# Performance work log

Measured on AMD Instinct MI355X. Metric: run time of the kernel, lower is better.

## Reference

```python
import jax, jax.numpy as jnp
import numpy as np
from jax import lax

B, N, S, C_IN, C_OUT = 4, 16384, 4096, 256, 256


def setup_inputs() -> dict:
    key = jax.random.key(0)
    k1, k2, k3, k4 = jax.random.split(key, 4)
    xyz1 = jax.random.normal(k1, (B, 3, N), dtype=jnp.float32)
    xyz2 = jax.random.normal(k2, (B, 3, S), dtype=jnp.float32)
    points2 = jax.random.normal(k3, (B, C_IN, S), dtype=jnp.float32)
    W = jax.random.normal(k4, (C_OUT, C_IN), dtype=jnp.float32) * (1.0 / np.sqrt(C_IN))
    b = jnp.zeros((C_OUT,), dtype=jnp.float32)
    return {"xyz1": xyz1, "xyz2": xyz2, "points2": points2, "W": W, "b": b}


def reference(xyz1, xyz2, points2, W, b):
    # channel-first -> channel-last
    p1 = jnp.transpose(xyz1, (0, 2, 1))        # [B, N, 3]
    p2 = jnp.transpose(xyz2, (0, 2, 1))        # [B, S, 3]
    f2 = jnp.transpose(points2, (0, 2, 1))     # [B, S, C]
    Bn, Nn, _ = p1.shape
    Cn = f2.shape[-1]
    # squared pairwise distances [B, N, S]
    d = (-2.0 * jnp.einsum('bnc,bsc->bns', p1, p2)
         + jnp.sum(p1 * p1, axis=-1)[:, :, None]
         + jnp.sum(p2 * p2, axis=-1)[:, None, :])
    # 3 nearest neighbors (smallest distances) -- equivalent to sort + slice :3
    neg_d3, idx = lax.top_k(-d, 3)             # [B, N, 3]
    d3 = -neg_d3
    recip = 1.0 / (d3 + 1e-8)
    weight = recip / jnp.sum(recip, axis=-1, keepdims=True)   # [B, N, 3]
    # gather neighbor features: [B, N, 3, C]
    gathered = jnp.take_along_axis(
        f2, idx.reshape(Bn, Nn * 3)[..., None], axis=1
    ).reshape(Bn, Nn, 3, Cn)
    interp = jnp.sum(gathered * weight[..., None], axis=2)    # [B, N, C]
    # Conv1d(kernel=1) == per-point linear: [B, C_out, N]
    out = jnp.einsum('bnc,oc->bon', interp, W) + b[None, :, None]
    return out
```

## Files before the change

### kernel.cpp

```cpp
#include <hip/hip_runtime.h>

#define BB 4
#define NN 16384
#define SS 4096
#define CIN 256
#define COUT 256

#define SC 8
#define SCS (SS / SC)
#define SUBS 16
#define SUBL 256
#define KNNB ((NN / 512) * SC * BB)
#define GEMMB ((COUT / 64) * (SS / 64) * BB)
#define RSLVB (BB * NN / 64)

typedef float v2f __attribute__((ext_vector_type(2)));
typedef float v4f __attribute__((ext_vector_type(4)));

__device__ __forceinline__ unsigned short f2bf(float f) {
    unsigned u = __float_as_uint(f);
    u += 0x7FFF + ((u >> 16) & 1);
    return (unsigned short)(u >> 16);
}
__device__ __forceinline__ float bf2f(unsigned short h) {
    return __uint_as_float((unsigned)h << 16);
}

__device__ __forceinline__ void ins_v(float e, float& a, float& b, float& c) {
    float n1 = __builtin_amdgcn_fmed3f(e, a, b);
    float n2 = __builtin_amdgcn_fmed3f(e, b, c);
    a = fminf(a, e); b = n1; c = n2;
}

__device__ __forceinline__ void insert_vi(float e, int gi,
                                          float& k0, float& k1, float& k2,
                                          int& i0, int& i1, int& i2) {
    bool c0 = e < k0, c1 = e < k1, c2 = e < k2;
    float n0 = fminf(e, k0);
    float n1 = __builtin_amdgcn_fmed3f(e, k0, k1);
    float n2 = __builtin_amdgcn_fmed3f(e, k1, k2);
    int t1 = c0 ? i0 : gi;
    int t2 = c1 ? i1 : gi;
    i0 = c0 ? gi : i0;
    i1 = c1 ? t1 : i1;
    i2 = c2 ? t2 : i2;
    k0 = n0; k1 = n1; k2 = n2;
}

__device__ __forceinline__ void ins_lex(float e, int gi,
                                        float& k0, float& k1, float& k2,
                                        int& i0, int& i1, int& i2) {
    bool c0 = (e < k0) || (e == k0 && gi < i0);
    bool c1 = (e < k1) || (e == k1 && gi < i1);
    bool c2 = (e < k2) || (e == k2 && gi < i2);
    float n0 = fminf(e, k0);
    float n1 = __builtin_amdgcn_fmed3f(e, k0, k1);
    float n2 = __builtin_amdgcn_fmed3f(e, k1, k2);
    int t1 = c0 ? i0 : gi;
    int t2 = c1 ? i1 : gi;
    i0 = c0 ? gi : i0;
    i1 = c1 ? t1 : i1;
    i2 = c2 ? t2 : i2;
    k0 = n0; k1 = n1; k2 = n2;
}

__device__ __forceinline__ int ltc(unsigned long long m) {
    return __builtin_amdgcn_mbcnt_hi(
        (unsigned)(m >> 32), __builtin_amdgcn_mbcnt_lo((unsigned)m, 0));
}

#define E2_FROM(p_xy, p_zw, XX, YY, ZZ, e2)                                    \
    do {                                                                       \
        asm("v_pk_fma_f32 %0, %1, %2, %3 op_sel:[0,0,1] op_sel_hi:[0,1,1]"     \
            : "=v"(e2) : "v"(p_zw), "v"(ZZ), "v"(p_zw));                       \
        asm("v_pk_fma_f32 %0, %1, %2, %0 op_sel:[1,0,0] op_sel_hi:[1,1,1]"     \
            : "+v"(e2) : "v"(p_xy), "v"(YY));                                  \
        asm("v_pk_fma_f32 %0, %1, %2, %0 op_sel:[0,0,0] op_sel_hi:[0,1,1]"     \
            : "+v"(e2) : "v"(p_xy), "v"(XX));                                  \
    } while (0)

#define PK_LO(acc, ap, bw)                                                     \
    asm("v_pk_fma_f32 %0, %1, %2, %0 op_sel:[0,0,0] op_sel_hi:[0,1,1]"         \
        : "+v"(acc) : "v"(ap), "v"(bw))
#define PK_HI(acc, ap, bw)                                                     \
    asm("v_pk_fma_f32 %0, %1, %2, %0 op_sel:[1,0,0] op_sel_hi:[1,1,1]"         \
        : "+v"(acc) : "v"(ap), "v"(bw))

__device__ __forceinline__ void knn_phase(int id, int t, float* smem,
                                          const float* __restrict__ xyz1,
                                          const float* __restrict__ xyz2,
                                          float* __restrict__ pv,
                                          float4* __restrict__ cand4) {
    int nb = id & 31;
    int ch = (id >> 5) & 7;
    int b  = id >> 8;
    int s0 = ch * SCS;

    float4* smv = (float4*)smem;
    const float* x2 = xyz2 + (size_t)b * 3 * SS;
    for (int i = t; i < SCS; i += 256) {
        float px = x2[s0 + i];
        float py = x2[SS + s0 + i];
        float pz = x2[2 * SS + s0 + i];
        float4 p4 = make_float4(px, py, pz, fmaf(px, px, fmaf(py, py, pz * pz)));
        smv[i] = p4;
        if (nb == 0) cand4[(size_t)b * SS + s0 + i] = p4;
    }
    __syncthreads();

    int n0  = nb * 512 + t;
    int n1q = n0 + 256;
    const float* xb = xyz1 + (size_t)b * 3 * NN;
    float ax = xb[n0],  ay = xb[NN + n0],  az = xb[2 * NN + n0];
    float bx = xb[n1q], by = xb[NN + n1q], bz = xb[2 * NN + n1q];
    v2f XX = {-2.0f * ax, -2.0f * bx};
    v2f YY = {-2.0f * ay, -2.0f * by};
    v2f ZZ = {-2.0f * az, -2.0f * bz};

#pragma unroll
    for (int half = 0; half < 2; ++half) {
        float A0 = 1e30f, A1 = 1e30f, A2 = 1e30f;
        float B0 = 1e30f, B1 = 1e30f, B2 = 1e30f;
        int sb = half * SUBL;
#pragma unroll 8
        for (int s = sb; s < sb + SUBL; ++s) {
            v4f p = *(const v4f*)(smem + 4 * s);
            v2f pxy = __builtin_shufflevector(p, p, 0, 1);
            v2f pzw = __builtin_shufflevector(p, p, 2, 3);
            v2f e2;
            E2_FROM(pxy, pzw, XX, YY, ZZ, e2);
            float nA1 = __builtin_amdgcn_fmed3f(e2.x, A0, A1);
            float nA2 = __builtin_amdgcn_fmed3f(e2.x, A1, A2);
            A0 = fminf(A0, e2.x); A1 = nA1; A2 = nA2;
            float nB1 = __builtin_amdgcn_fmed3f(e2.y, B0, B1);
            float nB2 = __builtin_amdgcn_fmed3f(e2.y, B1, B2);
            B0 = fminf(B0, e2.y); B1 = nB1; B2 = nB2;
        }
        int sub = ch * 2 + half;
        size_t base = (size_t)(sub * BB + b) * 3;
        pv[(base + 0) * NN + n0]  = A0;
        pv[(base + 1) * NN + n0]  = A1;
        pv[(base + 2) * NN + n0]  = A2;
        pv[(base + 0) * NN + n1q] = B0;
        pv[(base + 1) * NN + n1q] = B1;
        pv[(base + 2) * NN + n1q] = B2;
    }
}

__device__ __forceinline__ void gemm_phase(int g, int t, float* smem,
                                           const float* __restrict__ P,
                                           const float* __restrict__ W,
                                           const float* __restrict__ bias,
                                           unsigned short* __restrict__ Gh) {
    int o0 = (g & 3) * 64;
    int s0 = ((g >> 2) & 63) * 64;
    int b  = g >> 8;
    float* sP = smem;
    float* sW = smem + 1024;
    int i = t & 15;
    int j = t >> 4;

    v2f acc2[4][2];
#pragma unroll
    for (int p = 0; p < 4; ++p) {
        acc2[p][0] = (v2f){0.f, 0.f};
        acc2[p][1] = (v2f){0.f, 0.f};
    }

    const float* Pb = P + (size_t)b * CIN * SS;

    for (int c0 = 0; c0 < CIN; c0 += 16) {
        __syncthreads();
        {
            int col = t & 63;
            int r0r = t >> 6;
#pragma unroll
            for (int r = 0; r < 4; ++r) {
                int row = r0r + r * 4;
                sP[row * 64 + col] = Pb[(size_t)(c0 + row) * SS + s0 + col];
            }
        }
        {
            int cc = t & 15;
            int obase = t >> 4;
#pragma unroll
            for (int r = 0; r < 4; ++r) {
                int oo = obase + 16 * r;
                sW[cc * 68 + oo] = W[(size_t)(o0 + oo) * CIN + c0 + cc];
            }
        }
        __syncthreads();

#pragma unroll
        for (int cc = 0; cc < 16; ++cc) {
            v4f a  = *(const v4f*)&sP[cc * 64 + i * 4];
            v4f bv = *(const v4f*)&sW[cc * 68 + j * 4];
            v2f a01 = __builtin_shufflevector(a, a, 0, 1);
            v2f a23 = __builtin_shufflevector(a, a, 2, 3);
            v2f b01 = __builtin_shufflevector(bv, bv, 0, 1);
            v2f b23 = __builtin_shufflevector(bv, bv, 2, 3);
            PK_LO(acc2[0][0], a01, b01); PK_LO(acc2[0][1], a01, b23);
            PK_HI(acc2[1][0], a01, b01); PK_HI(acc2[1][1], a01, b23);
            PK_LO(acc2[2][0], a23, b01); PK_LO(acc2[2][1], a23, b23);
            PK_HI(acc2[3][0], a23, b01); PK_HI(acc2[3][1], a23, b23);
        }
    }

    float b0 = bias[o0 + j * 4 + 0];
    float b1 = bias[o0 + j * 4 + 1];
    float b2 = bias[o0 + j * 4 + 2];
    float b3 = bias[o0 + j * 4 + 3];
#pragma unroll
    for (int p = 0; p < 4; ++p) {
        ushort4 v;
        v.x = f2bf(acc2[p][0].x + b0);
        v.y = f2bf(acc2[p][0].y + b1);
        v.z = f2bf(acc2[p][1].x + b2);
        v.w = f2bf(acc2[p][1].y + b3);
        size_t off = ((size_t)b * SS + s0 + i * 4 + p) * COUT + o0 + j * 4;
        *(ushort4*)&Gh[off] = v;
    }
}

__global__ __launch_bounds__(256) void k_fused(const float* __restrict__ xyz1,
                                               const float* __restrict__ xyz2,
                                               const float* __restrict__ P,
                                               const float* __restrict__ W,
                                               const float* __restrict__ bias,
                                               unsigned short* __restrict__ Gh,
                                               float* __restrict__ pv,
                                               float4* __restrict__ cand4) {
    __shared__ float smem[2112];
    int bid = blockIdx.x;
    int t   = threadIdx.x;

    if (bid < KNNB) {
        knn_phase(bid, t, smem, xyz1, xyz2, pv, cand4);
    } else {
        gemm_phase(bid - KNNB, t, smem, P, W, bias, Gh);
    }
}

__global__ __launch_bounds__(256) void k_resolve(const float* __restrict__ pv,
                                                 const float* __restrict__ xyz1,
                                                 const float4* __restrict__ cand4,
                                                 float4* __restrict__ wi4,
                                                 int4* __restrict__ gi4) {
    __shared__ float    sv[4][64][3];
    __shared__ float    sj0[16][64];
    __shared__ float    sm2[64];
    __shared__ unsigned smask[64];
    __shared__ float    sq[64][4];
    __shared__ uint2    sl[4][16];
    int bid = blockIdx.x;
    int b   = bid >> 8;
    int n0  = (bid & 255) * 64;
    int t   = threadIdx.x;
    int w   = t >> 6;
    int l   = t & 63;

    const float* xb = xyz1 + (size_t)b * 3 * NN;

    {
        float a0 = 1e30f, a1 = 1e30f, a2 = 1e30f;
#pragma unroll
        for (int i = 0; i < 12; ++i) {
            int sub = w * 4 + i / 3;
            int j   = i % 3;
            float v = pv[((size_t)(sub * BB + b) * 3 + j) * NN + n0 + l];
            if (j == 0) sj0[sub][l] = v;
            ins_v(v, a0, a1, a2);
        }
        sv[w][l][0] = a0; sv[w][l][1] = a1; sv[w][l][2] = a2;
    }
    if (w == 1) {
        float qx = xb[n0 + l], qy = xb[NN + n0 + l], qz = xb[2 * NN + n0 + l];
        sq[l][0] = -2.0f * qx;
        sq[l][1] = -2.0f * qy;
        sq[l][2] = -2.0f * qz;
        sq[l][3] = fmaf(qx, qx, fmaf(qy, qy, qz * qz));
    }
    __syncthreads();

    {
        float m0 = 1e30f, m1 = 1e30f, m2 = 1e30f;
#pragma unroll
        for (int ww = 0; ww < 4; ++ww) {
            ins_v(sv[ww][l][0], m0, m1, m2);
            ins_v(sv[ww][l][1], m0, m1, m2);
            ins_v(sv[ww][l][2], m0, m1, m2);
        }
        unsigned mk = 0;
#pragma unroll
        for (int sub = 0; sub < SUBS; ++sub)
            mk |= (sj0[sub][l] <= m2) ? (1u << sub) : 0u;
        if (w == 0) { sm2[l] = m2; smask[l] = mk; }
    }
    __syncthreads();

    const float4* cb = cand4 + (size_t)b * SS;
    for (int qq = 0; qq < 16; ++qq) {
        int q = w * 16 + qq;
        int n = n0 + q;
        float    m2q = sm2[q];
        unsigned mm  = smask[q];
        float xm2c = sq[q][0], ym2c = sq[q][1], zm2c = sq[q][2];

        float k0 = 1e30f, k1 = 1e30f, k2 = 1e30f;
        int   i0 = 0,     i1 = 0,     i2 = 0;
        unsigned msc = mm;
        while (msc) {
            int sub = __builtin_ctz(msc); msc &= msc - 1;
            int sb = sub * SUBL;
#pragma unroll
            for (int r = 0; r < 4; ++r) {
                int gi = sb + r * 64 + l;
                float4 p = cb[gi];
                float e = fmaf(p.x, xm2c, fmaf(p.y, ym2c, fmaf(p.z, zm2c, p.w)));
                insert_vi(e, gi, k0, k1, k2, i0, i1, i2);
            }
        }

        unsigned long long b0 = __ballot(k0 <= m2q);
        unsigned long long b1 = __ballot(k1 <= m2q);
        unsigned long long b2 = __ballot(k2 <= m2q);
        int p0 = __popcll(b0), p1 = __popcll(b1);
        int cnt3 = p0 + p1 + __popcll(b2);
        float K0 = 1e30f, K1 = 1e30f, K2 = 1e30f;
        int   I0 = 0,     I1 = 0,     I2 = 0;
        if (cnt3 <= 16) {
            if (k0 <= m2q) sl[w][ltc(b0)]           = make_uint2(__float_as_uint(k0), (unsigned)i0);
            if (k1 <= m2q) sl[w][p0 + ltc(b1)]      = make_uint2(__float_as_uint(k1), (unsigned)i1);
            if (k2 <= m2q) sl[w][p0 + p1 + ltc(b2)] = make_uint2(__float_as_uint(k2), (unsigned)i2);
            for (int j = 0; j < cnt3; ++j) {
                uint2 u = sl[w][j];
                ins_lex(__uint_as_float(u.x), (int)u.y, K0, K1, K2, I0, I1, I2);
            }
        } else {
            unsigned mf = mm;
            while (mf) {
                int sub = __builtin_ctz(mf); mf &= mf - 1;
                int sb = sub * SUBL;
                for (int s = 0; s < SUBL; ++s) {
                    float4 p = cb[sb + s];
                    float e = fmaf(p.x, xm2c, fmaf(p.y, ym2c, fmaf(p.z, zm2c, p.w)));
                    ins_lex(e, sb + s, K0, K1, K2, I0, I1, I2);
                }
            }
        }

        if (l == 0) {
            float nrm = sq[q][3];
            float d0 = K0 + nrm, d1 = K1 + nrm, d2 = K2 + nrm;
            float r0 = 1.0f / (d0 + 1e-8f);
            float r1 = 1.0f / (d1 + 1e-8f);
            float r2 = 1.0f / (d2 + 1e-8f);
            float inv = 1.0f / (r0 + r1 + r2);
            size_t oq = (size_t)b * NN + n;
            wi4[oq] = make_float4(r0 * inv, r1 * inv, r2 * inv, 0.f);
            gi4[oq] = make_int4(I0, I1, I2, 0);
        }
    }
}

__global__ __launch_bounds__(256) void k_out(const unsigned short* __restrict__ Gh,
                                             const float4* __restrict__ wi4,
                                             const int4* __restrict__ gi4,
                                             float* __restrict__ out) {
    __shared__ float  tile[64 * 68];
    __shared__ float4 swv[64];
    __shared__ int4   siv[64];
    int bid  = blockIdx.x;
    int x    = bid & 7;
    int b    = x >> 1;
    int local = (bid >> 3) + (x & 1) * 512;
    int nb   = local & 255;
    int oc   = local >> 8;
    int n0   = nb * 64;
    int o0   = oc * 64;
    int t    = threadIdx.x;
    int wave = t >> 6;
    int lane = t & 63;
    int qg   = lane >> 4;
    int c16  = lane & 15;

    if (t < 64) {
        size_t q = (size_t)b * NN + n0 + t;
        swv[t] = wi4[q];
        siv[t] = gi4[q];
    }
    __syncthreads();

    const unsigned short* Gb = Gh + (size_t)b * SS * COUT;

#pragma unroll
    for (int pass = 0; pass < 4; ++pass) {
        int q = pass * 16 + wave * 4 + qg;
        float4 wv = swv[q];
        int4   iv = siv[q];
        int co = o0 + c16 * 4;
        ushort4 a0 = *(const ushort4*)(Gb + (size_t)iv.x * COUT + co);
        ushort4 a1 = *(const ushort4*)(Gb + (size_t)iv.y * COUT + co);
        ushort4 a2 = *(const ushort4*)(Gb + (size_t)iv.z * COUT + co);
        float4 v;
        v.x = fmaf(wv.x, bf2f(a0.x), fmaf(wv.y, bf2f(a1.x), wv.z * bf2f(a2.x)));
        v.y = fmaf(wv.x, bf2f(a0.y), fmaf(wv.y, bf2f(a1.y), wv.z * bf2f(a2.y)));
        v.z = fmaf(wv.x, bf2f(a0.z), fmaf(wv.y, bf2f(a1.z), wv.z * bf2f(a2.z)));
        v.w = fmaf(wv.x, bf2f(a0.w), fmaf(wv.y, bf2f(a1.w), wv.z * bf2f(a2.w)));
        *(float4*)&tile[q * 68 + c16 * 4] = v;
    }
    __syncthreads();

    float* obase = out + ((size_t)b * COUT + o0) * NN + n0 + lane;
#pragma unroll
    for (int g = 0; g < 4; ++g) {
        int c = wave * 16 + g * 4;
        float4 v = *(const float4*)&tile[lane * 68 + c];
        obase[(size_t)(c + 0) * NN] = v.x;
        obase[(size_t)(c + 1) * NN] = v.y;
        obase[(size_t)(c + 2) * NN] = v.z;
        obase[(size_t)(c + 3) * NN] = v.w;
    }
}

extern "C" void kernel_launch(void* const* d_in, const int* in_sizes, int n_in,
                              void* d_out, int out_size, void* d_ws, size_t ws_size,
                              hipStream_t stream) {
    const float* xyz1    = (const float*)d_in[0];
    const float* xyz2    = (const float*)d_in[1];
    const float* points2 = (const float*)d_in[2];
    const float* W       = (const float*)d_in[3];
    const float* bias    = (const float*)d_in[4];
    float* out = (float*)d_out;

    char* ws = (char*)d_ws;
    float*          pv  = (float*)(ws);
    unsigned short* Gh  = (unsigned short*)(ws + 12582912);
    float4*         wi4 = (float4*)(ws + 20971520);
    int4*           gi4 = (int4*)(ws + 22020096);
    float4* cand4 = (float4*)((char*)d_out + 66846720);

    k_fused<<<dim3(KNNB + GEMMB), 256, 0, stream>>>(xyz1, xyz2, points2, W, bias,
                                                    Gh, pv, cand4);
    k_resolve<<<dim3(RSLVB), 256, 0, stream>>>(pv, xyz1, cand4, wi4, gi4);
    k_out<<<dim3(4096), 256, 0, stream>>>(Gh, wi4, gi4, out);
}
```

Measured before the change: 210.4 us.

## Refine KNN pruning mask to 64-candidate subchunks with per-chunk minima

The KNN pass now records the minimum distance for each 64-candidate subchunk, not only per 256-candidate subchunk, and writes these minima into a scratch region of the output buffer. The resolve kernel builds a 64-bit mask of subchunks whose minimum is within the third-best bound, and rescans only those 64-point chunks. The first three chunk loads are issued up front. This cuts the candidates re-examined during resolve, at the cost of extra min tracking in the KNN inner loop and extra global writes and reads of the minima array.

```diff
diff --git a/kernel.cpp b/kernel.cpp
--- a/kernel.cpp
+++ b/kernel.cpp
@@ -10,6 +10,7 @@
 #define SCS (SS / SC)
 #define SUBS 16
 #define SUBL 256
+#define FSUB 64
 #define KNNB ((NN / 512) * SC * BB)
 #define GEMMB ((COUT / 64) * (SS / 64) * BB)
 #define RSLVB (BB * NN / 64)
@@ -90,6 +91,7 @@
                                           const float* __restrict__ xyz1,
                                           const float* __restrict__ xyz2,
                                           float* __restrict__ pv,
+                                          float* __restrict__ pm,
                                           float4* __restrict__ cand4) {
     int nb = id & 31;
     int ch = (id >> 5) & 7;
@@ -122,19 +124,26 @@
         float A0 = 1e30f, A1 = 1e30f, A2 = 1e30f;
         float B0 = 1e30f, B1 = 1e30f, B2 = 1e30f;
         int sb = half * SUBL;
+#pragma unroll
+        for (int k64 = 0; k64 < 4; ++k64) {
+            float mA = 1e30f, mB = 1e30f;
 #pragma unroll 8
-        for (int s = sb; s < sb + SUBL; ++s) {
-            v4f p = *(const v4f*)(smem + 4 * s);
-            v2f pxy = __builtin_shufflevector(p, p, 0, 1);
-            v2f pzw = __builtin_shufflevector(p, p, 2, 3);
-            v2f e2;
-            E2_FROM(pxy, pzw, XX, YY, ZZ, e2);
-            float nA1 = __builtin_amdgcn_fmed3f(e2.x, A0, A1);
-            float nA2 = __builtin_amdgcn_fmed3f(e2.x, A1, A2);
-            A0 = fminf(A0, e2.x); A1 = nA1; A2 = nA2;
-            float nB1 = __builtin_amdgcn_fmed3f(e2.y, B0, B1);
-            float nB2 = __builtin_amdgcn_fmed3f(e2.y, B1, B2);
-            B0 = fminf(B0, e2.y); B1 = nB1; B2 = nB2;
+            for (int s2 = 0; s2 < 64; ++s2) {
+                int s = sb + k64 * 64 + s2;
+                v4f p = *(const v4f*)(smem + 4 * s);
+                v2f pxy = __builtin_shufflevector(p, p, 0, 1);
+                v2f pzw = __builtin_shufflevector(p, p, 2, 3);
+                v2f e2;
+                E2_FROM(pxy, pzw, XX, YY, ZZ, e2);
+                ins_v(e2.x, A0, A1, A2);
+                ins_v(e2.y, B0, B1, B2);
+                mA = fminf(mA, e2.x);
+                mB = fminf(mB, e2.y);
+            }
+            int sub64 = ch * 8 + half * 4 + k64;
+            size_t pb = (size_t)(sub64 * BB + b) * NN;
+            pm[pb + n0]  = mA;
+            pm[pb + n1q] = mB;
         }
         int sub = ch * 2 + half;
         size_t base = (size_t)(sub * BB + b) * 3;
@@ -229,27 +238,29 @@
                                                const float* __restrict__ bias,
                                                unsigned short* __restrict__ Gh,
                                                float* __restrict__ pv,
+                                               float* __restrict__ pm,
                                                float4* __restrict__ cand4) {
     __shared__ float smem[2112];
     int bid = blockIdx.x;
     int t   = threadIdx.x;
 
     if (bid < KNNB) {
-        knn_phase(bid, t, smem, xyz1, xyz2, pv, cand4);
+        knn_phase(bid, t, smem, xyz1, xyz2, pv, pm, cand4);
     } else {
         gemm_phase(bid - KNNB, t, smem, P, W, bias, Gh);
     }
 }
 
 __global__ __launch_bounds__(256) void k_resolve(const float* __restrict__ pv,
+                                                 const float* __restrict__ pm,
                                                  const float* __restrict__ xyz1,
                                                  const float4* __restrict__ cand4,
                                                  float4* __restrict__ wi4,
                                                  int4* __restrict__ gi4) {
     __shared__ float    sv[4][64][3];
-    __shared__ float    sj0[16][64];
+    __shared__ float    pmv[FSUB][65];
     __shared__ float    sm2[64];
-    __shared__ unsigned smask[64];
+    __shared__ unsigned long long smask[64];
     __shared__ float    sq[64][4];
     __shared__ uint2    sl[4][16];
     int bid = blockIdx.x;
@@ -268,10 +279,14 @@
             int sub = w * 4 + i / 3;
             int j   = i % 3;
             float v = pv[((size_t)(sub * BB + b) * 3 + j) * NN + n0 + l];
-            if (j == 0) sj0[sub][l] = v;
             ins_v(v, a0, a1, a2);
         }
         sv[w][l][0] = a0; sv[w][l][1] = a1; sv[w][l][2] = a2;
+    }
+#pragma unroll
+    for (int i = 0; i < 16; ++i) {
+        int sub = w * 16 + i;
+        pmv[sub][l] = pm[(size_t)(sub * BB + b) * NN + n0 + l];
     }
     if (w == 1) {
         float qx = xb[n0 + l], qy = xb[NN + n0 + l], qz = xb[2 * NN + n0 + l];
@@ -290,10 +305,10 @@
             ins_v(sv[ww][l][1], m0, m1, m2);
             ins_v(sv[ww][l][2], m0, m1, m2);
         }
-        unsigned mk = 0;
-#pragma unroll
-        for (int sub = 0; sub < SUBS; ++sub)
-            mk |= (sj0[sub][l] <= m2) ? (1u << sub) : 0u;
+        unsigned long long mk = 0;
+#pragma unroll
+        for (int sub = 0; sub < FSUB; ++sub)
+            mk |= (pmv[sub][l] <= m2) ? (1ull << sub) : 0ull;
         if (w == 0) { sm2[l] = m2; smask[l] = mk; }
     }
     __syncthreads();
@@ -302,22 +317,42 @@
     for (int qq = 0; qq < 16; ++qq) {
         int q = w * 16 + qq;
         int n = n0 + q;
-        float    m2q = sm2[q];
-        unsigned mm  = smask[q];
+        float m2q = sm2[q];
+        unsigned long long mm = smask[q];
         float xm2c = sq[q][0], ym2c = sq[q][1], zm2c = sq[q][2];
+
+        int cntw = __popcll(mm);
+        unsigned long long r1m = mm  & (mm  - 1);
+        unsigned long long r2m = r1m & (r1m - 1);
+        int su0 = __builtin_ctzll(mm);
+        int su1 = r1m ? __builtin_ctzll(r1m) : su0;
+        int su2 = r2m ? __builtin_ctzll(r2m) : su0;
+
+        float4 P0 = cb[su0 * 64 + l];
+        float4 P1 = cb[su1 * 64 + l];
+        float4 P2 = cb[su2 * 64 + l];
 
         float k0 = 1e30f, k1 = 1e30f, k2 = 1e30f;
         int   i0 = 0,     i1 = 0,     i2 = 0;
-        unsigned msc = mm;
-        while (msc) {
-            int sub = __builtin_ctz(msc); msc &= msc - 1;
-            int sb = sub * SUBL;
-#pragma unroll
-            for (int r = 0; r < 4; ++r) {
-                int gi = sb + r * 64 + l;
-                float4 p = cb[gi];
+        {
+            float e = fmaf(P0.x, xm2c, fmaf(P0.y, ym2c, fmaf(P0.z, zm2c, P0.w)));
+            insert_vi(e, su0 * 64 + l, k0, k1, k2, i0, i1, i2);
+        }
+        if (cntw > 1) {
+            float e = fmaf(P1.x, xm2c, fmaf(P1.y, ym2c, fmaf(P1.z, zm2c, P1.w)));
+            insert_vi(e, su1 * 64 + l, k0, k1, k2, i0, i1, i2);
+        }
+        if (cntw > 2) {
+            float e = fmaf(P2.x, xm2c, fmaf(P2.y, ym2c, fmaf(P2.z, zm2c, P2.w)));
+            insert_vi(e, su2 * 64 + l, k0, k1, k2, i0, i1, i2);
+        }
+        if (cntw > 3) {
+            unsigned long long msc = r2m & (r2m - 1);
+            while (msc) {
+                int sub = __builtin_ctzll(msc); msc &= msc - 1;
+                float4 p = cb[sub * 64 + l];
                 float e = fmaf(p.x, xm2c, fmaf(p.y, ym2c, fmaf(p.z, zm2c, p.w)));
-                insert_vi(e, gi, k0, k1, k2, i0, i1, i2);
+                insert_vi(e, sub * 64 + l, k0, k1, k2, i0, i1, i2);
             }
         }
 
@@ -337,14 +372,13 @@
                 ins_lex(__uint_as_float(u.x), (int)u.y, K0, K1, K2, I0, I1, I2);
             }
         } else {
-            unsigned mf = mm;
+            unsigned long long mf = mm;
             while (mf) {
-                int sub = __builtin_ctz(mf); mf &= mf - 1;
-                int sb = sub * SUBL;
-                for (int s = 0; s < SUBL; ++s) {
-                    float4 p = cb[sb + s];
+                int sub = __builtin_ctzll(mf); mf &= mf - 1;
+                for (int s = 0; s < 64; ++s) {
+                    float4 p = cb[sub * 64 + s];
                     float e = fmaf(p.x, xm2c, fmaf(p.y, ym2c, fmaf(p.z, zm2c, p.w)));
-                    ins_lex(e, sb + s, K0, K1, K2, I0, I1, I2);
+                    ins_lex(e, sub * 64 + s, K0, K1, K2, I0, I1, I2);
                 }
             }
         }
@@ -438,10 +472,11 @@
     unsigned short* Gh  = (unsigned short*)(ws + 12582912);
     float4*         wi4 = (float4*)(ws + 20971520);
     int4*           gi4 = (int4*)(ws + 22020096);
+    float*  pm    = (float*)((char*)d_out + 50069504);
     float4* cand4 = (float4*)((char*)d_out + 66846720);
 
     k_fused<<<dim3(KNNB + GEMMB), 256, 0, stream>>>(xyz1, xyz2, points2, W, bias,
-                                                    Gh, pv, cand4);
-    k_resolve<<<dim3(RSLVB), 256, 0, stream>>>(pv, xyz1, cand4, wi4, gi4);
+                                                    Gh, pv, pm, cand4);
+    k_resolve<<<dim3(RSLVB), 256, 0, stream>>>(pv, pm, xyz1, cand4, wi4, gi4);
     k_out<<<dim3(4096), 256, 0, stream>>>(Gh, wi4, gi4, out);
 }
```

Result: faster. 204.0 us (-3.0%).
